# Kernel tuning notes

Hardware: AMD Instinct MI355X
Metric: run time of the kernel (lower is better)

Reference implementation:

```python
import jax, jax.numpy as jnp
import numpy as np

N_NODES = 10000
N_EDGES = 320000


def _prop(x, src, dst, wn, n):
    # y_i = sum_{(j->i) in E} wn_e * x_j   (sparse L_hat @ x)
    return jax.ops.segment_sum(wn[:, None] * x[src], dst, num_segments=n)


def _cheb(x, W, b, src, dst, wn, n):
    # PyG ChebConv: out = sum_k T_k(L_hat) x @ W[k] + b, via Chebyshev recurrence
    K = W.shape[0]
    out = x @ W[0]
    if K > 1:
        tx1 = _prop(x, src, dst, wn, n)
        out = out + tx1 @ W[1]
        if K > 2:
            def step(carry, Wk):
                t_prev, t_cur, acc = carry
                t_next = 2.0 * _prop(t_cur, src, dst, wn, n) - t_prev
                return (t_cur, t_next, acc + t_next @ Wk), None
            (_, _, out), _ = jax.lax.scan(step, (x, tx1, out), W[2:])
    if b is not None:
        out = out + b
    return out


def _norm(edge_weight, src, dst, n):
    # sym-normalized scaled Laplacian with lambda_max=2: L_hat = -D^-1/2 A D^-1/2 (zero diag)
    deg = jax.ops.segment_sum(edge_weight, src, num_segments=n)
    deg_safe = jnp.where(deg > 0, deg, 1.0)
    dis = jnp.where(deg > 0, 1.0 / jnp.sqrt(deg_safe), 0.0)
    return -dis[src] * edge_weight * dis[dst]


def setup_inputs() -> dict:
    key = jax.random.key(0)
    ks = jax.random.split(key, 12)

    def xav(k, shape):
        fan_in, fan_out = shape[-2], shape[-1]
        std = float(np.sqrt(2.0 / (fan_in + fan_out)))
        return jax.random.normal(k, shape, dtype=jnp.float32) * std

    x = jax.random.normal(ks[0], (N_NODES, 2), dtype=jnp.float32)
    edge_index = jax.random.randint(ks[1], (2, N_EDGES), 0, N_NODES, dtype=jnp.int64)
    edge_weight = jax.random.uniform(ks[2], (N_EDGES,), dtype=jnp.float32)
    return {
        "x": x,
        "edge_index": edge_index,
        "edge_weight": edge_weight,
        "W1": xav(ks[3], (200, 2, 60)),
        "b1": jnp.zeros((60,), jnp.float32),
        "W2": xav(ks[4], (200, 60, 60)),
        "b2": jnp.zeros((60,), jnp.float32),
        "W3": xav(ks[5], (20, 60, 30)),
        "b3": jnp.zeros((30,), jnp.float32),
        "W4": xav(ks[6], (1, 30, 1)),
    }


def reference(x, edge_index, edge_weight, W1, b1, W2, b2, W3, b3, W4):
    n = x.shape[0]
    src, dst = edge_index[0], edge_index[1]
    wn = _norm(edge_weight, src, dst, n)
    h = jax.nn.silu(_cheb(x, W1, b1, src, dst, wn, n))
    h = jax.nn.silu(_cheb(h, W2, b2, src, dst, wn, n))
    h = jax.nn.silu(_cheb(h, W3, b3, src, dst, wn, n))
    h = _cheb(h, W4, None, src, dst, wn, n)
    return jax.nn.sigmoid(h)
```

## Files before the change

### kernel.cpp

```cpp
#include <hip/hip_runtime.h>
#include <math.h>

#define N_NODES 10000
#define N_EDGES 320000

__global__ void k_detect(const int* __restrict__ ei, int* __restrict__ flag) {
  __shared__ int any_nz;
  if (threadIdx.x == 0) any_nz = 0;
  __syncthreads();
  if (ei[2 * threadIdx.x + 1] != 0) atomicOr(&any_nz, 1);
  __syncthreads();
  if (threadIdx.x == 0) *flag = (any_nz == 0) ? 1 : 0;
}

__device__ __forceinline__ int2 load_edge(const int* __restrict__ ei, int e, int is64) {
  if (is64) return make_int2(ei[2 * e], ei[2 * N_EDGES + 2 * e]);
  return make_int2(ei[e], ei[N_EDGES + e]);
}


__global__ void k_init(float* __restrict__ deg, int* __restrict__ cnt) {
  int i = blockIdx.x * blockDim.x + threadIdx.x;
  if (i < N_NODES) { deg[i] = 0.f; cnt[i] = 0; }
}

__global__ void k_deg(const int* __restrict__ ei, const float* __restrict__ w,
                      const int* __restrict__ flag,
                      float* __restrict__ deg, int* __restrict__ cnt) {
  const int is64 = *flag;
  int e = blockIdx.x * blockDim.x + threadIdx.x;
  if (e < N_EDGES) {
    int2 sd = load_edge(ei, e, is64);
    atomicAdd(&deg[sd.x], w[e]);
    atomicAdd(&cnt[sd.y], 1);
  }
}

__global__ __launch_bounds__(1024) void k_scan(const float* __restrict__ deg,
                                               float* __restrict__ dis,
                                               const int* __restrict__ cnt,
                                               int* __restrict__ row_ptr,
                                               int* __restrict__ cur) {
  __shared__ int sbuf[1024];
  const int tid = threadIdx.x;
  for (int i = tid; i < N_NODES; i += 1024) {
    float d = deg[i];
    dis[i] = d > 0.f ? 1.f / sqrtf(d) : 0.f;
    cur[i] = 0;
  }
  __syncthreads();
  int run = 0;
  for (int base = 0; base < N_NODES; base += 1024) {
    int v = (base + tid < N_NODES) ? cnt[base + tid] : 0;
    sbuf[tid] = v;
    __syncthreads();
    for (int o = 1; o < 1024; o <<= 1) {
      int t = (tid >= o) ? sbuf[tid - o] : 0;
      __syncthreads();
      sbuf[tid] += t;
      __syncthreads();
    }
    if (base + tid < N_NODES) row_ptr[base + tid + 1] = run + sbuf[tid];
    int tot = sbuf[1023];
    __syncthreads();
    run += tot;
  }
  if (tid == 0) row_ptr[0] = 0;
}

__global__ void k_fill(const int* __restrict__ ei, const float* __restrict__ w,
                       const int* __restrict__ flag, const float* __restrict__ dis,
                       const int* __restrict__ row_ptr, int* __restrict__ cur,
                       int* __restrict__ col, float* __restrict__ val) {
  const int is64 = *flag;
  int e = blockIdx.x * blockDim.x + threadIdx.x;
  if (e < N_EDGES) {
    int2 sd = load_edge(ei, e, is64);
    int p = row_ptr[sd.y] + atomicAdd(&cur[sd.y], 1);
    col[p] = sd.x;
    val[p] = -dis[sd.x] * w[e] * dis[sd.y];
  }
}


template <int CIN, int COUT, bool FIRST, bool LAST>
__global__ __launch_bounds__(256) void k_cheb(
    const int* __restrict__ row_ptr, const int* __restrict__ col, const float* __restrict__ val,
    const float* __restrict__ t_cur,
    const float* __restrict__ t_prev,
    float* __restrict__ t_next,
    const float* __restrict__ Wk,
    const float* __restrict__ W0,
    const float* __restrict__ bias,
    float* __restrict__ acc,
    float* __restrict__ h_out)
{
  __shared__ float ts[4][(CIN > 4) ? CIN : 1];
  __shared__ float xs[4][(FIRST && CIN > 4) ? CIN : 1];
  const int wid = threadIdx.x >> 6, lane = threadIdx.x & 63;
  const int node = blockIdx.x * 4 + wid;
  const int start = row_ptr[node], end = row_ptr[node + 1];

  float t0 = 0.f, t1 = 0.f;

  if constexpr (CIN == 2) {
    float s0 = 0.f, s1 = 0.f;
    for (int e = start + lane; e < end; e += 64) {
      int c = col[e]; float wv = val[e];
      float2 v = *reinterpret_cast<const float2*>(t_cur + 2 * c);
      s0 += wv * v.x; s1 += wv * v.y;
    }
#pragma unroll
    for (int o = 32; o; o >>= 1) { s0 += __shfl_xor(s0, o); s1 += __shfl_xor(s1, o); }
    if constexpr (FIRST) { t0 = s0; t1 = s1; }
    else { t0 = 2.f * s0 - t_prev[2 * node]; t1 = 2.f * s1 - t_prev[2 * node + 1]; }
    if (lane < 2) t_next[2 * node + lane] = lane ? t1 : t0;
  } else {
    const int cl = (lane < CIN) ? lane : 0;
    float a0 = 0.f, a1 = 0.f, a2 = 0.f, a3 = 0.f;
    int e = start;
    for (; e + 3 < end; e += 4) {
      int c0 = col[e], c1 = col[e + 1], c2 = col[e + 2], c3 = col[e + 3];
      float w0 = val[e], w1 = val[e + 1], w2 = val[e + 2], w3 = val[e + 3];
      a0 += w0 * t_cur[c0 * CIN + cl];
      a1 += w1 * t_cur[c1 * CIN + cl];
      a2 += w2 * t_cur[c2 * CIN + cl];
      a3 += w3 * t_cur[c3 * CIN + cl];
    }
    for (; e < end; e++) a0 += val[e] * t_cur[col[e] * CIN + cl];
    float p = (a0 + a1) + (a2 + a3);
    float tn;
    if constexpr (FIRST) tn = p;
    else tn = 2.f * p - t_prev[node * CIN + cl];
    if (lane < CIN) {
      t_next[node * CIN + lane] = tn;
      ts[wid][lane] = tn;
      if constexpr (FIRST) xs[wid][lane] = t_cur[node * CIN + lane];
    }
  }
  __syncthreads();

  if (lane < COUT) {
    float sum;
    if constexpr (FIRST) sum = bias[lane];
    else sum = acc[node * COUT + lane];
    if constexpr (CIN == 2) {
      sum += t0 * Wk[lane] + t1 * Wk[COUT + lane];
      if constexpr (FIRST) {
        float x0 = t_cur[2 * node], x1 = t_cur[2 * node + 1];
        sum += x0 * W0[lane] + x1 * W0[COUT + lane];
      }
    } else {
#pragma unroll
      for (int c = 0; c < CIN; c++) sum += ts[wid][c] * Wk[c * COUT + lane];
      if constexpr (FIRST) {
#pragma unroll
        for (int c = 0; c < CIN; c++) sum += xs[wid][c] * W0[c * COUT + lane];
      }
    }
    if constexpr (LAST) {
      h_out[node * COUT + lane] = sum / (1.f + expf(-sum));
    } else {
      acc[node * COUT + lane] = sum;
    }
  }
}

__global__ __launch_bounds__(256) void k_out(const float* __restrict__ h3,
                                             const float* __restrict__ W4,
                                             float* __restrict__ out) {
  const int wid = threadIdx.x >> 6, lane = threadIdx.x & 63;
  const int node = blockIdx.x * 4 + wid;
  float v = (lane < 30) ? h3[node * 30 + lane] * W4[lane] : 0.f;
#pragma unroll
  for (int o = 32; o; o >>= 1) v += __shfl_xor(v, o);
  if (lane == 0) out[node] = 1.f / (1.f + expf(-v));
}


template <int CI, int CO>
static void run_layer(const float* h_in, float* h_out, const float* W, const float* b, int K,
                      const int* rowp, const int* col, const float* val,
                      float* tA, float* tB, float* tC, float* accb, hipStream_t stream) {
  const int GB = N_NODES / 4;
  k_cheb<CI, CO, true, false><<<GB, 256, 0, stream>>>(rowp, col, val, h_in, nullptr, tA,
                                                      W + CI * CO, W, b, accb, nullptr);
  float* ptrs[3] = {tA, tB, tC};
  for (int k = 2; k < K; k++) {
    const float* prev = (k == 2) ? h_in : ptrs[(k - 3) % 3];
    const float* cur  = ptrs[(k - 2) % 3];
    float* next       = ptrs[(k - 1) % 3];
    if (k < K - 1)
      k_cheb<CI, CO, false, false><<<GB, 256, 0, stream>>>(rowp, col, val, cur, prev, next,
                                                           W + (size_t)k * CI * CO, nullptr,
                                                           nullptr, accb, nullptr);
    else
      k_cheb<CI, CO, false, true><<<GB, 256, 0, stream>>>(rowp, col, val, cur, prev, next,
                                                          W + (size_t)k * CI * CO, nullptr,
                                                          nullptr, accb, h_out);
  }
}

extern "C" void kernel_launch(void* const* d_in, const int* in_sizes, int n_in,
                              void* d_out, int out_size, void* d_ws, size_t ws_size,
                              hipStream_t stream) {
  const float* x  = (const float*)d_in[0];
  const int*   ei = (const int*)d_in[1];
  const float* ew = (const float*)d_in[2];
  const float* W1 = (const float*)d_in[3];
  const float* b1 = (const float*)d_in[4];
  const float* W2 = (const float*)d_in[5];
  const float* b2 = (const float*)d_in[6];
  const float* W3 = (const float*)d_in[7];
  const float* b3 = (const float*)d_in[8];
  const float* W4 = (const float*)d_in[9];
  float* out = (float*)d_out;

  char* ws = (char*)d_ws;
  size_t off = 0;
  auto alloc = [&](size_t bytes) {
    void* p = ws + off;
    off += (bytes + 255) & ~size_t(255);
    return p;
  };
  float* deg  = (float*)alloc(N_NODES * 4);
  float* dis  = (float*)alloc(N_NODES * 4);
  int*   cnt  = (int*)alloc(N_NODES * 4);
  int*   cur  = (int*)alloc(N_NODES * 4);
  int*   rowp = (int*)alloc((N_NODES + 1) * 4);
  int*   col  = (int*)alloc(N_EDGES * 4);
  float* val  = (float*)alloc(N_EDGES * 4);
  int*   flag = (int*)alloc(256);
  float* tA   = (float*)alloc(N_NODES * 60 * 4);
  float* tB   = (float*)alloc(N_NODES * 60 * 4);
  float* tC   = (float*)alloc(N_NODES * 60 * 4);
  float* accb = (float*)alloc(N_NODES * 60 * 4);
  float* h1   = (float*)alloc(N_NODES * 60 * 4);
  float* h2   = (float*)alloc(N_NODES * 60 * 4);
  float* h3   = (float*)alloc(N_NODES * 30 * 4);

  k_detect<<<1, 256, 0, stream>>>(ei, flag);
  k_init<<<(N_NODES + 255) / 256, 256, 0, stream>>>(deg, cnt);
  k_deg<<<(N_EDGES + 255) / 256, 256, 0, stream>>>(ei, ew, flag, deg, cnt);
  k_scan<<<1, 1024, 0, stream>>>(deg, dis, cnt, rowp, cur);
  k_fill<<<(N_EDGES + 255) / 256, 256, 0, stream>>>(ei, ew, flag, dis, rowp, cur, col, val);

  run_layer<2, 60>(x, h1, W1, b1, 200, rowp, col, val, tA, tB, tC, accb, stream);
  run_layer<60, 60>(h1, h2, W2, b2, 200, rowp, col, val, tA, tB, tC, accb, stream);
  run_layer<60, 30>(h2, h3, W3, b3, 20, rowp, col, val, tA, tB, tC, accb, stream);
  k_out<<<N_NODES / 4, 256, 0, stream>>>(h3, W4, out);
}
```

Baseline: 5.695 ms.

## Interleave CSR edges, pad feature rows to 64, transpose weights for vector loads

Packs each edge's column index and weight into one int2 so the SpMV reads one 8-byte record per edge, using 16-byte loads for pairs of edges. Pads the per-node feature buffers to a stride of 64 floats so gathered rows are aligned. Adds a kernel that transposes each weight matrix once per call, letting the dense W_k product read float4 rows. The block-wide __syncthreads becomes a wave barrier, since each wave owns its node. The cost is a larger workspace and three extra transpose launches per call.

```diff
diff --git a/kernel.cpp b/kernel.cpp
--- a/kernel.cpp
+++ b/kernel.cpp
@@ -71,95 +71,133 @@
 __global__ void k_fill(const int* __restrict__ ei, const float* __restrict__ w,
                        const int* __restrict__ flag, const float* __restrict__ dis,
                        const int* __restrict__ row_ptr, int* __restrict__ cur,
-                       int* __restrict__ col, float* __restrict__ val) {
+                       int2* __restrict__ edat) {
   const int is64 = *flag;
   int e = blockIdx.x * blockDim.x + threadIdx.x;
   if (e < N_EDGES) {
     int2 sd = load_edge(ei, e, is64);
     int p = row_ptr[sd.y] + atomicAdd(&cur[sd.y], 1);
-    col[p] = sd.x;
-    val[p] = -dis[sd.x] * w[e] * dis[sd.y];
-  }
-}
-
-
-template <int CIN, int COUT, bool FIRST, bool LAST>
+    float v = -dis[sd.x] * w[e] * dis[sd.y];
+    edat[p] = make_int2(sd.x, __float_as_int(v));
+  }
+}
+
+__global__ void k_tr(const float* __restrict__ W, float* __restrict__ Wt,
+                     int K, int CI, int CO) {
+  int i = blockIdx.x * blockDim.x + threadIdx.x;
+  int tot = K * CI * CO;
+  if (i < tot) {
+    int k = i / (CI * CO), r = i % (CI * CO);
+    int ci = r / CO, co = r % CO;
+    Wt[k * CI * CO + co * CI + ci] = W[i];
+  }
+}
+
+
+template <int CIN, int COUT, int SIN, bool FIRST, bool LAST>
 __global__ __launch_bounds__(256) void k_cheb(
-    const int* __restrict__ row_ptr, const int* __restrict__ col, const float* __restrict__ val,
+    const int* __restrict__ row_ptr, const int2* __restrict__ edat,
     const float* __restrict__ t_cur,
     const float* __restrict__ t_prev,
+    int sprev,
     float* __restrict__ t_next,
-    const float* __restrict__ Wk,
-    const float* __restrict__ W0,
+    const float* __restrict__ Wkt,
+    const float* __restrict__ W0t,
     const float* __restrict__ bias,
     float* __restrict__ acc,
     float* __restrict__ h_out)
 {
-  __shared__ float ts[4][(CIN > 4) ? CIN : 1];
-  __shared__ float xs[4][(FIRST && CIN > 4) ? CIN : 1];
+  constexpr int ST = (CIN == 2) ? 2 : 64;
+  constexpr int SCUR = FIRST ? SIN : ST;
+  __shared__ __align__(16) float ts[4][(CIN > 4) ? 64 : 1];
+  __shared__ __align__(16) float xs[4][(FIRST && CIN > 4) ? 64 : 1];
   const int wid = threadIdx.x >> 6, lane = threadIdx.x & 63;
   const int node = blockIdx.x * 4 + wid;
   const int start = row_ptr[node], end = row_ptr[node + 1];
 
-  float t0 = 0.f, t1 = 0.f;
+  float tn0 = 0.f, tn1 = 0.f;
 
   if constexpr (CIN == 2) {
     float s0 = 0.f, s1 = 0.f;
     for (int e = start + lane; e < end; e += 64) {
-      int c = col[e]; float wv = val[e];
-      float2 v = *reinterpret_cast<const float2*>(t_cur + 2 * c);
+      int2 ed = edat[e];
+      float wv = __int_as_float(ed.y);
+      float2 v = *reinterpret_cast<const float2*>(t_cur + ed.x * SCUR);
       s0 += wv * v.x; s1 += wv * v.y;
     }
 #pragma unroll
     for (int o = 32; o; o >>= 1) { s0 += __shfl_xor(s0, o); s1 += __shfl_xor(s1, o); }
-    if constexpr (FIRST) { t0 = s0; t1 = s1; }
-    else { t0 = 2.f * s0 - t_prev[2 * node]; t1 = 2.f * s1 - t_prev[2 * node + 1]; }
-    if (lane < 2) t_next[2 * node + lane] = lane ? t1 : t0;
+    if constexpr (FIRST) { tn0 = s0; tn1 = s1; }
+    else {
+      tn0 = 2.f * s0 - t_prev[node * sprev];
+      tn1 = 2.f * s1 - t_prev[node * sprev + 1];
+    }
+    if (lane == 0) *reinterpret_cast<float2*>(t_next + node * ST) = make_float2(tn0, tn1);
   } else {
     const int cl = (lane < CIN) ? lane : 0;
     float a0 = 0.f, a1 = 0.f, a2 = 0.f, a3 = 0.f;
     int e = start;
+    if (e < end && (e & 1)) {
+      int2 ed = edat[e];
+      a0 += __int_as_float(ed.y) * t_cur[ed.x * SCUR + cl];
+      e++;
+    }
     for (; e + 3 < end; e += 4) {
-      int c0 = col[e], c1 = col[e + 1], c2 = col[e + 2], c3 = col[e + 3];
-      float w0 = val[e], w1 = val[e + 1], w2 = val[e + 2], w3 = val[e + 3];
-      a0 += w0 * t_cur[c0 * CIN + cl];
-      a1 += w1 * t_cur[c1 * CIN + cl];
-      a2 += w2 * t_cur[c2 * CIN + cl];
-      a3 += w3 * t_cur[c3 * CIN + cl];
-    }
-    for (; e < end; e++) a0 += val[e] * t_cur[col[e] * CIN + cl];
+      int4 p0 = *reinterpret_cast<const int4*>(edat + e);
+      int4 p1 = *reinterpret_cast<const int4*>(edat + e + 2);
+      a0 += __int_as_float(p0.y) * t_cur[p0.x * SCUR + cl];
+      a1 += __int_as_float(p0.w) * t_cur[p0.z * SCUR + cl];
+      a2 += __int_as_float(p1.y) * t_cur[p1.x * SCUR + cl];
+      a3 += __int_as_float(p1.w) * t_cur[p1.z * SCUR + cl];
+    }
+    for (; e < end; e++) {
+      int2 ed = edat[e];
+      a0 += __int_as_float(ed.y) * t_cur[ed.x * SCUR + cl];
+    }
     float p = (a0 + a1) + (a2 + a3);
     float tn;
     if constexpr (FIRST) tn = p;
-    else tn = 2.f * p - t_prev[node * CIN + cl];
+    else tn = 2.f * p - t_prev[node * sprev + cl];
     if (lane < CIN) {
-      t_next[node * CIN + lane] = tn;
+      t_next[node * ST + lane] = tn;
       ts[wid][lane] = tn;
-      if constexpr (FIRST) xs[wid][lane] = t_cur[node * CIN + lane];
-    }
-  }
-  __syncthreads();
+      if constexpr (FIRST) xs[wid][lane] = t_cur[node * SIN + lane];
+    }
+    __builtin_amdgcn_wave_barrier();
+  }
 
   if (lane < COUT) {
     float sum;
     if constexpr (FIRST) sum = bias[lane];
     else sum = acc[node * COUT + lane];
     if constexpr (CIN == 2) {
-      sum += t0 * Wk[lane] + t1 * Wk[COUT + lane];
+      const float2 wk = *reinterpret_cast<const float2*>(Wkt + lane * 2);
+      sum += tn0 * wk.x + tn1 * wk.y;
       if constexpr (FIRST) {
-        float x0 = t_cur[2 * node], x1 = t_cur[2 * node + 1];
-        sum += x0 * W0[lane] + x1 * W0[COUT + lane];
+        const float2 w0 = *reinterpret_cast<const float2*>(W0t + lane * 2);
+        float x0 = t_cur[node * SIN], x1 = t_cur[node * SIN + 1];
+        sum += x0 * w0.x + x1 * w0.y;
       }
     } else {
-#pragma unroll
-      for (int c = 0; c < CIN; c++) sum += ts[wid][c] * Wk[c * COUT + lane];
+      const float4* wrow = reinterpret_cast<const float4*>(Wkt + lane * CIN);
+#pragma unroll
+      for (int c4 = 0; c4 < CIN / 4; c4++) {
+        float4 w = wrow[c4];
+        float4 t = *reinterpret_cast<const float4*>(&ts[wid][c4 * 4]);
+        sum += w.x * t.x + w.y * t.y + w.z * t.z + w.w * t.w;
+      }
       if constexpr (FIRST) {
-#pragma unroll
-        for (int c = 0; c < CIN; c++) sum += xs[wid][c] * W0[c * COUT + lane];
+        const float4* w0row = reinterpret_cast<const float4*>(W0t + lane * CIN);
+#pragma unroll
+        for (int c4 = 0; c4 < CIN / 4; c4++) {
+          float4 w = w0row[c4];
+          float4 t = *reinterpret_cast<const float4*>(&xs[wid][c4 * 4]);
+          sum += w.x * t.x + w.y * t.y + w.z * t.z + w.w * t.w;
+        }
       }
     }
     if constexpr (LAST) {
-      h_out[node * COUT + lane] = sum / (1.f + expf(-sum));
+      h_out[node * 64 + lane] = sum / (1.f + expf(-sum));
     } else {
       acc[node * COUT + lane] = sum;
     }
@@ -171,33 +209,36 @@
                                              float* __restrict__ out) {
   const int wid = threadIdx.x >> 6, lane = threadIdx.x & 63;
   const int node = blockIdx.x * 4 + wid;
-  float v = (lane < 30) ? h3[node * 30 + lane] * W4[lane] : 0.f;
+  float v = (lane < 30) ? h3[node * 64 + lane] * W4[lane] : 0.f;
 #pragma unroll
   for (int o = 32; o; o >>= 1) v += __shfl_xor(v, o);
   if (lane == 0) out[node] = 1.f / (1.f + expf(-v));
 }
 
 
-template <int CI, int CO>
-static void run_layer(const float* h_in, float* h_out, const float* W, const float* b, int K,
-                      const int* rowp, const int* col, const float* val,
+template <int CI, int CO, int SIN>
+static void run_layer(const float* h_in, float* h_out, const float* Wt, const float* b, int K,
+                      const int* rowp, const int2* edat,
                       float* tA, float* tB, float* tC, float* accb, hipStream_t stream) {
   const int GB = N_NODES / 4;
-  k_cheb<CI, CO, true, false><<<GB, 256, 0, stream>>>(rowp, col, val, h_in, nullptr, tA,
-                                                      W + CI * CO, W, b, accb, nullptr);
+  constexpr int ST = (CI == 2) ? 2 : 64;
+  (void)ST;
+  k_cheb<CI, CO, SIN, true, false><<<GB, 256, 0, stream>>>(
+      rowp, edat, h_in, nullptr, 0, tA, Wt + CI * CO, Wt, b, accb, nullptr);
   float* ptrs[3] = {tA, tB, tC};
   for (int k = 2; k < K; k++) {
     const float* prev = (k == 2) ? h_in : ptrs[(k - 3) % 3];
+    int sprev = (k == 2) ? SIN : ST;
     const float* cur  = ptrs[(k - 2) % 3];
     float* next       = ptrs[(k - 1) % 3];
     if (k < K - 1)
-      k_cheb<CI, CO, false, false><<<GB, 256, 0, stream>>>(rowp, col, val, cur, prev, next,
-                                                           W + (size_t)k * CI * CO, nullptr,
-                                                           nullptr, accb, nullptr);
+      k_cheb<CI, CO, SIN, false, false><<<GB, 256, 0, stream>>>(
+          rowp, edat, cur, prev, sprev, next, Wt + (size_t)k * CI * CO, nullptr, nullptr,
+          accb, nullptr);
     else
-      k_cheb<CI, CO, false, true><<<GB, 256, 0, stream>>>(rowp, col, val, cur, prev, next,
-                                                          W + (size_t)k * CI * CO, nullptr,
-                                                          nullptr, accb, h_out);
+      k_cheb<CI, CO, SIN, false, true><<<GB, 256, 0, stream>>>(
+          rowp, edat, cur, prev, sprev, next, Wt + (size_t)k * CI * CO, nullptr, nullptr,
+          accb, h_out);
   }
 }
 
@@ -228,25 +269,31 @@
   int*   cnt  = (int*)alloc(N_NODES * 4);
   int*   cur  = (int*)alloc(N_NODES * 4);
   int*   rowp = (int*)alloc((N_NODES + 1) * 4);
-  int*   col  = (int*)alloc(N_EDGES * 4);
-  float* val  = (float*)alloc(N_EDGES * 4);
+  int2*  edat = (int2*)alloc(N_EDGES * 8);
   int*   flag = (int*)alloc(256);
-  float* tA   = (float*)alloc(N_NODES * 60 * 4);
-  float* tB   = (float*)alloc(N_NODES * 60 * 4);
-  float* tC   = (float*)alloc(N_NODES * 60 * 4);
+  float* Wt1  = (float*)alloc(200 * 2 * 60 * 4);
+  float* Wt2  = (float*)alloc(200 * 60 * 60 * 4);
+  float* Wt3  = (float*)alloc(20 * 60 * 30 * 4);
+  float* tA   = (float*)alloc(N_NODES * 64 * 4);
+  float* tB   = (float*)alloc(N_NODES * 64 * 4);
+  float* tC   = (float*)alloc(N_NODES * 64 * 4);
   float* accb = (float*)alloc(N_NODES * 60 * 4);
-  float* h1   = (float*)alloc(N_NODES * 60 * 4);
-  float* h2   = (float*)alloc(N_NODES * 60 * 4);
-  float* h3   = (float*)alloc(N_NODES * 30 * 4);
+  float* h1   = (float*)alloc(N_NODES * 64 * 4);
+  float* h2   = (float*)alloc(N_NODES * 64 * 4);
+  float* h3   = (float*)alloc(N_NODES * 64 * 4);
 
   k_detect<<<1, 256, 0, stream>>>(ei, flag);
   k_init<<<(N_NODES + 255) / 256, 256, 0, stream>>>(deg, cnt);
   k_deg<<<(N_EDGES + 255) / 256, 256, 0, stream>>>(ei, ew, flag, deg, cnt);
   k_scan<<<1, 1024, 0, stream>>>(deg, dis, cnt, rowp, cur);
-  k_fill<<<(N_EDGES + 255) / 256, 256, 0, stream>>>(ei, ew, flag, dis, rowp, cur, col, val);
-
-  run_layer<2, 60>(x, h1, W1, b1, 200, rowp, col, val, tA, tB, tC, accb, stream);
-  run_layer<60, 60>(h1, h2, W2, b2, 200, rowp, col, val, tA, tB, tC, accb, stream);
-  run_layer<60, 30>(h2, h3, W3, b3, 20, rowp, col, val, tA, tB, tC, accb, stream);
+  k_fill<<<(N_EDGES + 255) / 256, 256, 0, stream>>>(ei, ew, flag, dis, rowp, cur, edat);
+
+  k_tr<<<(200 * 2 * 60 + 255) / 256, 256, 0, stream>>>(W1, Wt1, 200, 2, 60);
+  k_tr<<<(200 * 60 * 60 + 255) / 256, 256, 0, stream>>>(W2, Wt2, 200, 60, 60);
+  k_tr<<<(20 * 60 * 30 + 255) / 256, 256, 0, stream>>>(W3, Wt3, 20, 60, 30);
+
+  run_layer<2, 60, 2>(x, h1, Wt1, b1, 200, rowp, edat, tA, tB, tC, accb, stream);
+  run_layer<60, 60, 64>(h1, h2, Wt2, b2, 200, rowp, edat, tA, tB, tC, accb, stream);
+  run_layer<60, 30, 64>(h2, h3, Wt3, b3, 20, rowp, edat, tA, tB, tC, accb, stream);
   k_out<<<N_NODES / 4, 256, 0, stream>>>(h3, W4, out);
 }
```

Measured after the change: 6.030 ms. 1.06x slower.
